# Optimization experiments

Measured on AMD Instinct MI355X. Metric: run time of the kernel, lower is better.

## Reference

```python
import jax, jax.numpy as jnp
import numpy as np

B, DIM, HEADS, H, W = 2, 256, 8, 40, 40


def setup_inputs() -> dict:
    key = jax.random.key(0)
    ks = jax.random.split(key, 11)
    s = 0.05
    return {
        "x": jax.random.normal(ks[0], (B, DIM, H, W), jnp.float32),
        "qkv_w": jax.random.normal(ks[1], (3 * DIM, DIM, 1, 1), jnp.float32) * s,
        "qkv_b": jax.random.normal(ks[2], (3 * DIM,), jnp.float32) * s,
        "pos_w": jax.random.normal(ks[3], (3 * DIM, 1, 3, 3), jnp.float32) * s,
        "pos_b": jax.random.normal(ks[4], (3 * DIM,), jnp.float32) * s,
        "proj_w": jax.random.normal(ks[5], (DIM, DIM), jnp.float32) * s,
        "proj_b": jax.random.normal(ks[6], (DIM,), jnp.float32) * s,
        "g1_w": jax.random.normal(ks[7], (16, 1), jnp.float32),
        "g1_b": jax.random.normal(ks[8], (16,), jnp.float32),
        "g2_w": jax.random.normal(ks[9], (1, 16), jnp.float32),
        "g2_b": jax.random.normal(ks[10], (1,), jnp.float32),
    }


def _conv(x, w, b, groups=1, pad=0):
    # NCHW conv, OIHW weights (matches torch Conv2d)
    y = jax.lax.conv_general_dilated(x, w, (1, 1), [(pad, pad), (pad, pad)],
                                     feature_group_count=groups)
    return y + b[None, :, None, None]


def reference(x, qkv_w, qkv_b, pos_w, pos_b, proj_w, proj_b, g1_w, g1_b, g2_w, g2_b):
    b, c, h, w = x.shape
    n = h * w
    hd = c // HEADS
    scale = hd ** -0.5

    qkv = _conv(x, qkv_w, qkv_b)                     # [b, 3c, h, w]
    qkv = _conv(qkv, pos_w, pos_b, groups=3 * c, pad=1)  # depthwise 3x3
    q, k, v = jnp.split(qkv, 3, axis=1)

    def to_heads(t):  # [b,c,h,w] -> [b, heads, n, head_dim]
        return t.reshape(b, HEADS, hd, n).transpose(0, 1, 3, 2)

    q, k, v = to_heads(q), to_heads(k), to_heads(v)

    attn = jnp.einsum('bhnd,bhmd->bhnm', q, k) * scale      # [b,H,n,n]
    prob = jax.nn.softmax(attn, axis=-1)
    entropy = -(prob * jnp.log(jnp.clip(prob, 1e-12))).sum(-1).mean(-1)  # [b,H]

    # EntropyGate: ratio in [0.1, 1.0]
    hid = jax.nn.relu(entropy[..., None] @ g1_w.T + g1_b)
    ratio = jax.nn.sigmoid(hid @ g2_w.T + g2_b)[..., 0] * 0.9 + 0.1      # [b,H]

    # dynamic per-(b,head) top-k: keep = ceil(ratio*n), clamped to [1,n]
    keep = jnp.clip(jnp.ceil(ratio * n).astype(jnp.int32), 1, n)          # [b,H]
    srt = jnp.flip(jnp.sort(attn, axis=-1), axis=-1)                      # descending
    idx = jnp.broadcast_to((keep - 1)[:, :, None, None], (b, HEADS, n, 1))
    kth = jnp.take_along_axis(srt, idx, axis=-1)                          # [b,H,n,1]
    sparse = jnp.where(attn >= kth, attn, -jnp.inf)

    p = jax.nn.softmax(sparse, axis=-1)
    out = jnp.einsum('bhnm,bhmd->bhnd', p, v)
    out = out.transpose(0, 2, 1, 3).reshape(b, n, c)
    out = out @ proj_w.T + proj_b
    return out.transpose(0, 2, 1).reshape(b, c, h, w)
```

## Files before the change

### kernel.cpp

```cpp
#include <hip/hip_runtime.h>
#include <math.h>

#define BB 2
#define CDIM 256
#define NHEADS 8
#define HD 32
#define HH 40
#define WW 40
#define NN 1600
#define C3 768
#define SCALE 0.17677669529663687f
#define RTE 8
#define RTS 2
#define TSTR 2048
#define HSTR 51200

__device__ inline unsigned fkey(float f) {
    unsigned u = __float_as_uint(f);
    return (u & 0x80000000u) ? ~u : (u | 0x80000000u);
}
__device__ inline float finv(unsigned u) {
    unsigned v = (u & 0x80000000u) ? (u ^ 0x80000000u) : ~u;
    return __uint_as_float(v);
}

__global__ __launch_bounds__(256) void conv1x1_kernel(const float* __restrict__ x,
                                                      const float* __restrict__ w,
                                                      const float* __restrict__ bias,
                                                      float* __restrict__ out) {
    int blk = blockIdx.x;
    int st = blk % 7;
    int t2 = blk / 7;
    int ocg = t2 % (C3 / 8);
    int b = t2 / (C3 / 8);
    int s = st * 256 + threadIdx.x;
    if (s >= NN) return;
    int oc0 = ocg * 8;
    const float* xb = x + (size_t)b * CDIM * NN + s;
    const float* w0 = w + (size_t)oc0 * CDIM;
    float a[8];
#pragma unroll
    for (int i = 0; i < 8; i++) a[i] = bias[oc0 + i];
#pragma unroll 4
    for (int ic = 0; ic < CDIM; ic++) {
        float xv = xb[(size_t)ic * NN];
#pragma unroll
        for (int i = 0; i < 8; i++) a[i] += w0[i * CDIM + ic] * xv;
    }
    float* ob = out + ((size_t)b * C3 + oc0) * NN + s;
#pragma unroll
    for (int i = 0; i < 8; i++) ob[(size_t)i * NN] = a[i];
}

__global__ __launch_bounds__(256) void dwconv_kernel(const float* __restrict__ in,
                                                     const float* __restrict__ w,
                                                     const float* __restrict__ bias,
                                                     float* __restrict__ out_t) {
    int idx = blockIdx.x * 256 + threadIdx.x;
    int s = idx % NN;
    int t = idx / NN;
    int c = t % C3;
    int b = t / C3;
    int y = s / WW, xx = s % WW;
    const float* ib = in + ((size_t)b * C3 + c) * NN;
    const float* wr = w + (size_t)c * 9;
    float acc = bias[c];
#pragma unroll
    for (int ky = 0; ky < 3; ky++) {
        int iy = y + ky - 1;
        if (iy < 0 || iy >= HH) continue;
#pragma unroll
        for (int kx = 0; kx < 3; kx++) {
            int ix = xx + kx - 1;
            if (ix < 0 || ix >= WW) continue;
            acc += wr[ky * 3 + kx] * ib[iy * WW + ix];
        }
    }
    int part = c >> 8;
    int r = c & 255;
    int hh = r >> 5;
    int d = r & 31;
    out_t[((size_t)(b * 3 + part) * NHEADS + hh) * HSTR + (s >> 6) * TSTR + d * 64 + (s & 63)] = acc;
}

__global__ __launch_bounds__(256) void entropy_kernel(const float* __restrict__ qkv_t,
                                                      float* __restrict__ ent) {
    int blk = blockIdx.x;
    int rt = blk % (NN / RTE);
    int bh = blk / (NN / RTE);
    int h = bh % NHEADS, b = bh / NHEADS;
    int row0 = rt * RTE;
    __shared__ float Qs[RTE][HD];
    int tid = threadIdx.x;
    const float* qt = qkv_t + ((size_t)(b * 3 + 0) * NHEADS + h) * HSTR;
    const float* ktb = qkv_t + ((size_t)(b * 3 + 1) * NHEADS + h) * HSTR;
    {
        int r = tid >> 5, d = tid & 31;
        int row = row0 + r;
        Qs[r][d] = qt[(row >> 6) * TSTR + d * 64 + (row & 63)];
    }
    __syncthreads();
    int w = tid >> 6, lane = tid & 63;
    int lr0 = 2 * w, lr1 = lr0 + 1;
    float q0[HD], q1[HD];
#pragma unroll
    for (int d = 0; d < HD; d++) { q0[d] = Qs[lr0][d]; q1[d] = Qs[lr1][d]; }
    float S0 = 0.f, T0 = 0.f, S1 = 0.f, T1 = 0.f;
#pragma unroll 1
    for (int kt = 0; kt < 25; kt++) {
        const float* kp = ktb + kt * TSTR + lane;
        float a0 = 0.f, a1 = 0.f;
#pragma unroll
        for (int dc = 0; dc < 4; dc++) {
            float kc[8];
#pragma unroll
            for (int i = 0; i < 8; i++) kc[i] = kp[(dc * 8 + i) * 64];
#pragma unroll
            for (int i = 0; i < 8; i++) {
                a0 += q0[dc * 8 + i] * kc[i];
                a1 += q1[dc * 8 + i] * kc[i];
            }
        }
        a0 *= SCALE; a1 *= SCALE;
        float e0 = __expf(a0), e1 = __expf(a1);
        S0 += e0; T0 += e0 * a0;
        S1 += e1; T1 += e1 * a1;
    }
#pragma unroll
    for (int o = 1; o < 64; o <<= 1) {
        S0 += __shfl_xor(S0, o); T0 += __shfl_xor(T0, o);
        S1 += __shfl_xor(S1, o); T1 += __shfl_xor(T1, o);
    }
    if (lane == 0) {
        ent[(size_t)bh * NN + row0 + lr0] = logf(S0) - T0 / S0;
        ent[(size_t)bh * NN + row0 + lr1] = logf(S1) - T1 / S1;
    }
}

__global__ void gate_kernel(const float* __restrict__ ent_rows,
                            const float* __restrict__ g1w, const float* __restrict__ g1b,
                            const float* __restrict__ g2w, const float* __restrict__ g2b,
                            int* __restrict__ keep) {
    int bh = blockIdx.x;
    int tid = threadIdx.x;
    __shared__ float red[4];
    float ls = 0.f;
    for (int j = tid; j < NN; j += 256) ls += ent_rows[bh * NN + j];
    for (int o = 32; o > 0; o >>= 1) ls += __shfl_down(ls, o);
    int lane = tid & 63, wid = tid >> 6;
    if (lane == 0) red[wid] = ls;
    __syncthreads();
    if (tid == 0) {
        float ent = (red[0] + red[1] + red[2] + red[3]) / (float)NN;
        float val = g2b[0];
#pragma unroll
        for (int j = 0; j < 16; j++) {
            float hid = ent * g1w[j] + g1b[j];
            if (hid < 0.f) hid = 0.f;
            val += hid * g2w[j];
        }
        float ratio = 0.9f / (1.f + expf(-val)) + 0.1f;
        int kp = (int)ceilf(ratio * (float)NN);
        if (kp < 1) kp = 1;
        if (kp > NN) kp = NN;
        keep[bh] = kp;
    }
}

__global__ __launch_bounds__(64) void sparse_attn_kernel(const float* __restrict__ qkv_t,
                                                         const int* __restrict__ keep,
                                                         float* __restrict__ oht) {
    int blk = blockIdx.x;
    int rt = blk % (NN / RTS);
    int bh = blk / (NN / RTS);
    int h = bh % NHEADS, b = bh / NHEADS;
    int row0 = rt * RTS;
    __shared__ float att[RTS][NN];
    __shared__ unsigned hist[RTS][256];
    __shared__ float Qs[RTS][HD];
    int tid = threadIdx.x;
    const float* qt = qkv_t + ((size_t)(b * 3 + 0) * NHEADS + h) * HSTR;
    const float* ktb = qkv_t + ((size_t)(b * 3 + 1) * NHEADS + h) * HSTR;
    const float* vtb = qkv_t + ((size_t)(b * 3 + 2) * NHEADS + h) * HSTR;
    {
        int r = tid >> 5, d = tid & 31;
        int row = row0 + r;
        Qs[r][d] = qt[(row >> 6) * TSTR + d * 64 + (row & 63)];
    }
    int want = keep[bh];
    __syncthreads();
    int lane = tid;
    float q0[HD], q1[HD];
#pragma unroll
    for (int d = 0; d < HD; d++) { q0[d] = Qs[0][d]; q1[d] = Qs[1][d]; }

    float m0 = -1e30f, m1 = -1e30f;
    for (int kt = 0; kt < 25; kt++) {
        const float* kp = ktb + kt * TSTR + lane;
        int j = kt * 64 + lane;
        float kc[HD];
#pragma unroll
        for (int d = 0; d < HD; d++) kc[d] = kp[d * 64];
        float a0 = 0.f, a1 = 0.f;
#pragma unroll
        for (int d = 0; d < HD; d++) { a0 += q0[d] * kc[d]; a1 += q1[d] * kc[d]; }
        a0 *= SCALE; a1 *= SCALE;
        att[0][j] = a0;
        att[1][j] = a1;
        m0 = fmaxf(m0, a0); m1 = fmaxf(m1, a1);
    }
#pragma unroll
    for (int off = 1; off < 64; off <<= 1) {
        m0 = fmaxf(m0, __shfl_xor(m0, off));
        m1 = fmaxf(m1, __shfl_xor(m1, off));
    }

    int l = lane & 31;
    int r = (lane < 32) ? 0 : 1;
    unsigned kvr[50];
#pragma unroll
    for (int k2 = 0; k2 < 50; k2++) kvr[k2] = fkey(att[r][k2 * 32 + l]);

    unsigned prefixHigh = 0;
    for (int pass = 0; pass < 4; pass++) {
        int shift = 24 - 8 * pass;
#pragma unroll
        for (int i = 0; i < 8; i++) hist[r][248 - 8 * l + i] = 0u;
#pragma unroll
        for (int k2 = 0; k2 < 50; k2++) {
            unsigned u = kvr[k2];
            bool ok = (pass == 0) || ((u >> (shift + 8)) == prefixHigh);
            if (ok) atomicAdd(&hist[r][(u >> shift) & 255u], 1u);
        }
        unsigned sch = 0;
#pragma unroll
        for (int i = 0; i < 8; i++) sch += hist[r][248 - 8 * l + i];
        unsigned inc = sch;
#pragma unroll
        for (int dlt = 1; dlt < 32; dlt <<= 1) {
            unsigned tv = __shfl_up(inc, dlt, 32);
            if (l >= dlt) inc += tv;
        }
        unsigned pref = inc - sch;
        bool found = (pref < (unsigned)want) && ((unsigned)want <= inc);
        int bsel = -1, wnew = 0;
        if (found) {
            unsigned want2 = (unsigned)want - pref, cum = 0;
#pragma unroll
            for (int i = 0; i < 8; i++) {
                int bbin = 255 - 8 * l - i;
                unsigned c = hist[r][bbin];
                if (bsel < 0 && cum + c >= want2) { bsel = bbin; wnew = (int)(want2 - cum); }
                cum += c;
            }
        }
        unsigned long long mk = __ballot(found);
        int src = (lane < 32) ? __builtin_ctzll(mk & 0xffffffffULL)
                              : __builtin_ctzll(mk >> 32) + 32;
        bsel = __shfl(bsel, src);
        want = __shfl(wnew, src);
        prefixHigh = (prefixHigh << 8) | (unsigned)bsel;
    }
    float kth = finv(prefixHigh);
    float kth0 = __shfl(kth, 0);
    float kth1 = __shfl(kth, 32);

    float acc0[HD], acc1[HD];
#pragma unroll
    for (int d = 0; d < HD; d++) { acc0[d] = 0.f; acc1[d] = 0.f; }
    float S0 = 0.f, S1 = 0.f;
    for (int kt = 0; kt < 25; kt++) {
        const float* vp = vtb + kt * TSTR + lane;
        int j = kt * 64 + lane;
        float a0 = att[0][j];
        float a1 = att[1][j];
        float p0 = (a0 >= kth0) ? __expf(a0 - m0) : 0.f;
        float p1 = (a1 >= kth1) ? __expf(a1 - m1) : 0.f;
        S0 += p0; S1 += p1;
#pragma unroll
        for (int d = 0; d < HD; d++) {
            float vv = vp[d * 64];
            acc0[d] += p0 * vv;
            acc1[d] += p1 * vv;
        }
    }
#pragma unroll
    for (int off = 1; off < 64; off <<= 1) {
        S0 += __shfl_xor(S0, off);
        S1 += __shfl_xor(S1, off);
    }

    float* scratch = &att[0][0];
    int dd = lane & 31;
    int jb = (lane < 32) ? 0 : 32;
#pragma unroll
    for (int d = 0; d < HD; d++) scratch[lane * 33 + d] = acc0[d];
    float sum0 = 0.f;
#pragma unroll
    for (int jj = 0; jj < 32; jj++) sum0 += scratch[(jb + jj) * 33 + dd];
    sum0 += __shfl_xor(sum0, 32);
#pragma unroll
    for (int d = 0; d < HD; d++) scratch[lane * 33 + d] = acc1[d];
    float sum1 = 0.f;
#pragma unroll
    for (int jj = 0; jj < 32; jj++) sum1 += scratch[(jb + jj) * 33 + dd];
    sum1 += __shfl_xor(sum1, 32);

    if (lane < 32) {
        size_t base = ((size_t)b * CDIM + h * HD + dd) * NN + row0;
        oht[base + 0] = sum0 / S0;
        oht[base + 1] = sum1 / S1;
    }
}

__global__ __launch_bounds__(256) void proj_kernel(const float* __restrict__ oht,
                                                   const float* __restrict__ pw,
                                                   const float* __restrict__ pb,
                                                   float* __restrict__ out) {
    int blk = blockIdx.x;
    int st = blk % 7;
    int t2 = blk / 7;
    int ocg = t2 % (CDIM / 8);
    int b = t2 / (CDIM / 8);
    int s = st * 256 + threadIdx.x;
    if (s >= NN) return;
    int co0 = ocg * 8;
    const float* ib = oht + (size_t)b * CDIM * NN + s;
    const float* w0 = pw + (size_t)co0 * CDIM;
    float a[8];
#pragma unroll
    for (int i = 0; i < 8; i++) a[i] = pb[co0 + i];
#pragma unroll 4
    for (int c = 0; c < CDIM; c++) {
        float xv = ib[(size_t)c * NN];
#pragma unroll
        for (int i = 0; i < 8; i++) a[i] += w0[i * CDIM + c] * xv;
    }
    float* ob = out + ((size_t)b * CDIM + co0) * NN + s;
#pragma unroll
    for (int i = 0; i < 8; i++) ob[(size_t)i * NN] = a[i];
}

extern "C" void kernel_launch(void* const* d_in, const int* in_sizes, int n_in,
                              void* d_out, int out_size, void* d_ws, size_t ws_size,
                              hipStream_t stream) {
    const float* x      = (const float*)d_in[0];
    const float* qkv_w  = (const float*)d_in[1];
    const float* qkv_b  = (const float*)d_in[2];
    const float* pos_w  = (const float*)d_in[3];
    const float* pos_b  = (const float*)d_in[4];
    const float* proj_w = (const float*)d_in[5];
    const float* proj_b = (const float*)d_in[6];
    const float* g1w    = (const float*)d_in[7];
    const float* g1b    = (const float*)d_in[8];
    const float* g2w    = (const float*)d_in[9];
    const float* g2b    = (const float*)d_in[10];
    float* out = (float*)d_out;

    float* ws   = (float*)d_ws;
    float* buf1 = ws;
    float* buf2 = buf1 + (size_t)BB * C3 * NN;
    float* ent  = buf2 + (size_t)BB * C3 * NN;
    float* oht  = ent + (size_t)BB * NHEADS * NN;
    int* keep   = (int*)(oht + (size_t)BB * CDIM * NN);

    conv1x1_kernel<<<BB * (C3 / 8) * 7, 256, 0, stream>>>(x, qkv_w, qkv_b, buf1);
    dwconv_kernel<<<BB * C3 * NN / 256, 256, 0, stream>>>(buf1, pos_w, pos_b, buf2);
    entropy_kernel<<<NHEADS * BB * (NN / RTE), 256, 0, stream>>>(buf2, ent);
    gate_kernel<<<BB * NHEADS, 256, 0, stream>>>(ent, g1w, g1b, g2w, g2b, keep);
    sparse_attn_kernel<<<NHEADS * BB * (NN / RTS), 64, 0, stream>>>(buf2, keep, oht);
    proj_kernel<<<BB * (CDIM / 8) * 7, 256, 0, stream>>>(oht, proj_w, proj_b, out);
}
```

Baseline: 439.0 us.

## Store attention scores as fp16 keys, two-pass radix select, shuffle reduce-scatter

Attention scores are now stored in shared memory as 16-bit order-preserving fp16 keys instead of fp32. This halves LDS use and cuts the radix top-k threshold search from four histogram passes to two. The row-max pass is dropped, so softmax exponentiates the raw score without subtracting the max. The final cross-lane reduction uses a butterfly reduce-scatter of shuffles instead of an LDS transpose. The risks are fp16 rounding changing which scores pass the kth threshold (ties), and possible overflow or precision loss in exp without max subtraction.

New measurement: 1.096 ms. +149.5%, slower.

```diff
diff --git a/kernel.cpp b/kernel.cpp
--- a/kernel.cpp
+++ b/kernel.cpp
@@ -1,4 +1,5 @@
 #include <hip/hip_runtime.h>
+#include <hip/hip_fp16.h>
 #include <math.h>
 
 #define BB 2
@@ -15,13 +16,36 @@
 #define TSTR 2048
 #define HSTR 51200
 
-__device__ inline unsigned fkey(float f) {
-    unsigned u = __float_as_uint(f);
-    return (u & 0x80000000u) ? ~u : (u | 0x80000000u);
-}
-__device__ inline float finv(unsigned u) {
-    unsigned v = (u & 0x80000000u) ? (u ^ 0x80000000u) : ~u;
-    return __uint_as_float(v);
+__device__ inline unsigned short fkey16(unsigned short u) {
+    return (u & 0x8000) ? (unsigned short)(~u) : (unsigned short)(u | 0x8000);
+}
+__device__ inline float h16tof(unsigned short b) {
+    __half_raw r; r.x = b;
+    return __half2float(__half(r));
+}
+__device__ inline float keytof(unsigned short k) {
+    unsigned short v = (k & 0x8000) ? (unsigned short)(k ^ 0x8000) : (unsigned short)(~k);
+    return h16tof(v);
+}
+
+__device__ inline float reduce_scatter32(float (&v)[32], int lane) {
+#pragma unroll
+    for (int step = 0; step < 5; step++) {
+        const int off = 1 << step;
+        const bool up = (lane >> step) & 1;
+        const int h = 32 >> (step + 1);
+#pragma unroll
+        for (int i = 0; i < h; i++) {
+            float send = up ? v[i] : v[h + i];
+            float recv = __shfl_xor(send, off);
+            float keep = up ? v[h + i] : v[i];
+            v[i] = keep + recv;
+        }
+    }
+    return v[0] + __shfl_xor(v[0], 32);
+}
+__device__ inline int scatter_d(int lane) {
+    return ((lane & 1) << 4) | ((lane & 2) << 2) | (lane & 4) | ((lane >> 2) & 2) | ((lane >> 4) & 1);
 }
 
 __global__ __launch_bounds__(256) void conv1x1_kernel(const float* __restrict__ x,
@@ -175,9 +199,10 @@
     int bh = blk / (NN / RTS);
     int h = bh % NHEADS, b = bh / NHEADS;
     int row0 = rt * RTS;
-    __shared__ float att[RTS][NN];
+    __shared__ unsigned att16u[RTS * NN / 2];
     __shared__ unsigned hist[RTS][256];
     __shared__ float Qs[RTS][HD];
+    unsigned short* att16 = (unsigned short*)att16u;
     int tid = threadIdx.x;
     const float* qt = qkv_t + ((size_t)(b * 3 + 0) * NHEADS + h) * HSTR;
     const float* ktb = qkv_t + ((size_t)(b * 3 + 1) * NHEADS + h) * HSTR;
@@ -194,7 +219,6 @@
 #pragma unroll
     for (int d = 0; d < HD; d++) { q0[d] = Qs[0][d]; q1[d] = Qs[1][d]; }
 
-    float m0 = -1e30f, m1 = -1e30f;
     for (int kt = 0; kt < 25; kt++) {
         const float* kp = ktb + kt * TSTR + lane;
         int j = kt * 64 + lane;
@@ -205,32 +229,33 @@
 #pragma unroll
         for (int d = 0; d < HD; d++) { a0 += q0[d] * kc[d]; a1 += q1[d] * kc[d]; }
         a0 *= SCALE; a1 *= SCALE;
-        att[0][j] = a0;
-        att[1][j] = a1;
-        m0 = fmaxf(m0, a0); m1 = fmaxf(m1, a1);
-    }
-#pragma unroll
-    for (int off = 1; off < 64; off <<= 1) {
-        m0 = fmaxf(m0, __shfl_xor(m0, off));
-        m1 = fmaxf(m1, __shfl_xor(m1, off));
-    }
+        att16[j] = fkey16(__half_as_ushort(__float2half(a0)));
+        att16[NN + j] = fkey16(__half_as_ushort(__float2half(a1)));
+    }
+    __syncthreads();
 
     int l = lane & 31;
     int r = (lane < 32) ? 0 : 1;
-    unsigned kvr[50];
-#pragma unroll
-    for (int k2 = 0; k2 < 50; k2++) kvr[k2] = fkey(att[r][k2 * 32 + l]);
+    unsigned kvp[25];
+#pragma unroll
+    for (int i = 0; i < 25; i++) kvp[i] = att16u[r * (NN / 2) + i * 32 + l];
 
     unsigned prefixHigh = 0;
-    for (int pass = 0; pass < 4; pass++) {
-        int shift = 24 - 8 * pass;
+    for (int pass = 0; pass < 2; pass++) {
+        int shift = 8 - 8 * pass;
 #pragma unroll
         for (int i = 0; i < 8; i++) hist[r][248 - 8 * l + i] = 0u;
 #pragma unroll
-        for (int k2 = 0; k2 < 50; k2++) {
-            unsigned u = kvr[k2];
-            bool ok = (pass == 0) || ((u >> (shift + 8)) == prefixHigh);
-            if (ok) atomicAdd(&hist[r][(u >> shift) & 255u], 1u);
+        for (int i = 0; i < 25; i++) {
+            unsigned u = kvp[i];
+            unsigned k0 = u & 0xFFFFu, k1 = u >> 16;
+            if (pass == 0) {
+                atomicAdd(&hist[r][k0 >> 8], 1u);
+                atomicAdd(&hist[r][k1 >> 8], 1u);
+            } else {
+                if ((k0 >> 8) == prefixHigh) atomicAdd(&hist[r][k0 & 255u], 1u);
+                if ((k1 >> 8) == prefixHigh) atomicAdd(&hist[r][k1 & 255u], 1u);
+            }
         }
         unsigned sch = 0;
 #pragma unroll
@@ -260,10 +285,10 @@
         bsel = __shfl(bsel, src);
         want = __shfl(wnew, src);
         prefixHigh = (prefixHigh << 8) | (unsigned)bsel;
-    }
-    float kth = finv(prefixHigh);
-    float kth0 = __shfl(kth, 0);
-    float kth1 = __shfl(kth, 32);
+        (void)shift;
+    }
+    unsigned kb0 = (unsigned)__shfl((int)prefixHigh, 0);
+    unsigned kb1 = (unsigned)__shfl((int)prefixHigh, 32);
 
     float acc0[HD], acc1[HD];
 #pragma unroll
@@ -272,10 +297,10 @@
     for (int kt = 0; kt < 25; kt++) {
         const float* vp = vtb + kt * TSTR + lane;
         int j = kt * 64 + lane;
-        float a0 = att[0][j];
-        float a1 = att[1][j];
-        float p0 = (a0 >= kth0) ? __expf(a0 - m0) : 0.f;
-        float p1 = (a1 >= kth1) ? __expf(a1 - m1) : 0.f;
+        unsigned k0 = att16[j];
+        unsigned k1 = att16[NN + j];
+        float p0 = (k0 >= kb0) ? __expf(keytof((unsigned short)k0)) : 0.f;
+        float p1 = (k1 >= kb1) ? __expf(keytof((unsigned short)k1)) : 0.f;
         S0 += p0; S1 += p1;
 #pragma unroll
         for (int d = 0; d < HD; d++) {
@@ -290,26 +315,13 @@
         S1 += __shfl_xor(S1, off);
     }
 
-    float* scratch = &att[0][0];
-    int dd = lane & 31;
-    int jb = (lane < 32) ? 0 : 32;
-#pragma unroll
-    for (int d = 0; d < HD; d++) scratch[lane * 33 + d] = acc0[d];
-    float sum0 = 0.f;
-#pragma unroll
-    for (int jj = 0; jj < 32; jj++) sum0 += scratch[(jb + jj) * 33 + dd];
-    sum0 += __shfl_xor(sum0, 32);
-#pragma unroll
-    for (int d = 0; d < HD; d++) scratch[lane * 33 + d] = acc1[d];
-    float sum1 = 0.f;
-#pragma unroll
-    for (int jj = 0; jj < 32; jj++) sum1 += scratch[(jb + jj) * 33 + dd];
-    sum1 += __shfl_xor(sum1, 32);
-
+    float tot0 = reduce_scatter32(acc0, lane);
+    float tot1 = reduce_scatter32(acc1, lane);
+    int dd = scatter_d(lane);
     if (lane < 32) {
         size_t base = ((size_t)b * CDIM + h * HD + dd) * NN + row0;
-        oht[base + 0] = sum0 / S0;
-        oht[base + 1] = sum1 / S1;
+        oht[base + 0] = tot0 / S0;
+        oht[base + 1] = tot1 / S1;
     }
 }
 
```
